# Optimization experiments

Hardware: AMD Instinct MI355X
Metric: run time of the kernel (lower is better)

## Reference

```python
import math
import jax, jax.numpy as jnp
import numpy as np

B, S, G, D = 16, 256, 2048, 512
H = 8
DK = D // H  # per-head key dim
E = 8        # num experts
TOPK = 2


def setup_inputs() -> dict:
    key = jax.random.key(0)
    ks = jax.random.split(key, 12)
    init = lambda k, shape, fan_in: jax.random.uniform(k, shape, jnp.float32, -1.0, 1.0) / np.sqrt(fan_in)
    return {
        'query': jax.random.normal(ks[0], (B, S, D), jnp.float32),
        'key': jax.random.normal(ks[1], (B, G, D), jnp.float32),
        'value': jax.random.normal(ks[2], (B, G, D), jnp.float32),  # unused by module (MHA uses h=key)
        'logit_key': jax.random.normal(ks[3], (B, G, D), jnp.float32),
        'attn_mask': jnp.zeros((B, G), dtype=bool),
        'Wq': init(ks[4], (H, D, DK), D),
        'Wk': init(ks[5], (H, D, DK), D),
        'Wv': init(ks[6], (H, D, DK), D),
        'Wo': init(ks[7], (H, DK, D), DK),
        'w_gate': jnp.zeros((D, E), jnp.float32) + init(ks[8], (D, E), D) * 0.0 + init(ks[9], (D, E), D),
        'expert_w': init(ks[10], (E, D, D), D),
    }


def _mha_glimpse(query, h, attn_mask, Wq, Wk, Wv, Wo):
    # Kool-style MHA: K and V both derived from h
    Q = jnp.einsum('bsd,hdk->bhsk', query, Wq)
    K = jnp.einsum('bgd,hdk->bhgk', h, Wk)
    V = jnp.einsum('bgd,hdk->bhgk', h, Wv)
    scores = jnp.einsum('bhsk,bhgk->bhsg', Q, K) / math.sqrt(DK)
    # 2D mask (B,G) expanded over heads and steps; True = masked out
    mask = attn_mask[:, None, None, :]
    scores = jnp.where(mask, jnp.float32(-1e9), scores)
    attn = jax.nn.softmax(scores, axis=-1)
    heads = jnp.einsum('bhsg,bhgk->bhsk', attn, V)
    return jnp.einsum('bhsk,hkd->bsd', heads, Wo)


def _moe(x, w_gate, expert_w):
    # x: (N, D). Noisy top-k gating, eval mode (no noise): clean logits -> top-k -> softmax over top-k.
    logits = x @ w_gate                                  # (N, E)
    top_vals, top_idx = jax.lax.top_k(logits, TOPK)      # (N, k)
    top_gates = jax.nn.softmax(top_vals, axis=-1)        # (N, k)
    gates = jnp.sum(jax.nn.one_hot(top_idx, E, dtype=x.dtype) * top_gates[..., None], axis=1)  # (N, E)
    expert_out = jnp.einsum('nd,edo->neo', x, expert_w)  # dense combine: same math as dispatch/scatter
    return jnp.einsum('ne,neo->no', gates, expert_out)


def reference(query, key, value, logit_key, attn_mask, Wq, Wk, Wv, Wo, w_gate, expert_w):
    glimpse = _mha_glimpse(query, key, attn_mask, Wq, Wk, Wv, Wo)  # (B, S, D)
    gm = _moe(glimpse.reshape(B * S, D), w_gate, expert_w).reshape(B, S, D)
    logits = jnp.einsum('bsd,bgd->bsg', gm, logit_key) / math.sqrt(D)
    return logits
```

## Files before the change

kernel.cpp:

```cpp
#include <hip/hip_runtime.h>

#define B_  16
#define S_  256
#define G_  2048
#define D_  512
#define H_  8
#define DK_ 64
#define E_  8

typedef _Float16 half8  __attribute__((ext_vector_type(8)));
typedef _Float16 half4v __attribute__((ext_vector_type(4)));
typedef float    floatx4 __attribute__((ext_vector_type(4)));
typedef float    floatx16 __attribute__((ext_vector_type(16)));

#define GLDS(g, l) __builtin_amdgcn_global_load_lds( \
    (const __attribute__((address_space(1))) void*)(g), \
    (__attribute__((address_space(3))) void*)(l), 16, 0, 0)

__global__ void __launch_bounds__(256) split_f16(
    const float* __restrict__ src, _Float16* __restrict__ hi,
    _Float16* __restrict__ lo, int n4)
{
    int i = blockIdx.x * 256 + threadIdx.x;
    if (i >= n4) return;
    float4 v = ((const float4*)src)[i];
    half4v h, l;
    h[0] = (_Float16)v.x; h[1] = (_Float16)v.y;
    h[2] = (_Float16)v.z; h[3] = (_Float16)v.w;
    l[0] = (_Float16)(v.x - (float)h[0]); l[1] = (_Float16)(v.y - (float)h[1]);
    l[2] = (_Float16)(v.z - (float)h[2]); l[3] = (_Float16)(v.w - (float)h[3]);
    ((half4v*)hi)[i] = h;
    ((half4v*)lo)[i] = l;
}

__global__ void __launch_bounds__(256) transpose_split(
    const float* __restrict__ src, _Float16* __restrict__ hi,
    _Float16* __restrict__ lo, int R, int C)
{
    __shared__ float T[32][33];
    const int tid = threadIdx.x;
    const long zo = (long)blockIdx.z * R * C;
    const int r0 = blockIdx.y * 32, c0 = blockIdx.x * 32;
#pragma unroll
    for (int p = 0; p < 4; ++p) {
        int i = tid + p * 256;
        int lr = i >> 5, lc = i & 31;
        T[lr][lc] = src[zo + (long)(r0 + lr) * C + (c0 + lc)];
    }
    __syncthreads();
#pragma unroll
    for (int p = 0; p < 4; ++p) {
        int i = tid + p * 256;
        int orr = i >> 5, oc = i & 31;
        float v = T[oc][orr];
        _Float16 h = (_Float16)v;
        long o = zo + (long)(c0 + orr) * R + (r0 + oc);
        hi[o] = h;
        lo[o] = (_Float16)(v - (float)h);
    }
}

__global__ void __launch_bounds__(256) mask_bitmap(
    const unsigned char* __restrict__ mask, unsigned long long* __restrict__ bmp)
{
    const int t = blockIdx.x * 256 + threadIdx.x;
    const int b = t >> 5, tile = t & 31;
    const unsigned long long* m8 =
        (const unsigned long long*)(mask + (long)b * G_ + tile * 64);
    unsigned long long v = 0ULL;
#pragma unroll
    for (int i = 0; i < 8; ++i) {
        const unsigned long long w = m8[i];
#pragma unroll
        for (int j = 0; j < 8; ++j)
            v |= (((w >> (8 * j)) & 0xFFULL) ? 1ULL : 0ULL) << (8 * i + j);
    }
    bmp[t] = v;
}

__global__ void __launch_bounds__(256) gemm_f16x3(
    const _Float16* __restrict__ Ah, const _Float16* __restrict__ Al,
    const _Float16* __restrict__ Bh, const _Float16* __restrict__ Bl,
    float* __restrict__ C, _Float16* __restrict__ Chi, _Float16* __restrict__ Clo,
    long ldc, long sAz, long sBz, long sCz, float alpha)
{
    __shared__ _Float16 Ash[128 * 32], Asl[128 * 32];
    __shared__ _Float16 Bsh[128 * 32], Bsl[128 * 32];
    const int tid = threadIdx.x;
    const int w = tid >> 6, lane = tid & 63;
    const int quad = lane >> 4, tn = lane & 15;
    const int wm = (w >> 1) * 64, wn = (w & 1) * 64;
    const int z = blockIdx.z;
    const long m0 = (long)blockIdx.y * 128;
    const long n0 = (long)blockIdx.x * 128;
    const _Float16* Agh = Ah + (z * sAz + m0) * 512;
    const _Float16* Agl = Al + (z * sAz + m0) * 512;
    const _Float16* Bgh = Bh + (z * sBz + n0) * 512;
    const _Float16* Bgl = Bl + (z * sBz + n0) * 512;
    const long glane = (long)(lane >> 2) * 512 + (lane & 3) * 8;

    floatx4 acc[4][4] = {};

    for (int k0 = 0; k0 < 512; k0 += 32) {
#pragma unroll
        for (int cc = 0; cc < 2; ++cc) {
            const int c = 2 * w + cc;
            const long go = (long)c * 16 * 512 + glane + k0;
            GLDS(Agh + go, Ash + c * 512);
            GLDS(Agl + go, Asl + c * 512);
            GLDS(Bgh + go, Bsh + c * 512);
            GLDS(Bgl + go, Bsl + c * 512);
        }
        asm volatile("s_waitcnt vmcnt(0)" ::: "memory");
        __syncthreads();

        half8 ah[4], al[4], bh[4], bl[4];
#pragma unroll
        for (int t = 0; t < 4; ++t) {
            ah[t] = *(const half8*)&Ash[(wm + t * 16 + tn) * 32 + quad * 8];
            al[t] = *(const half8*)&Asl[(wm + t * 16 + tn) * 32 + quad * 8];
            bh[t] = *(const half8*)&Bsh[(wn + t * 16 + tn) * 32 + quad * 8];
            bl[t] = *(const half8*)&Bsl[(wn + t * 16 + tn) * 32 + quad * 8];
        }
#pragma unroll
        for (int i = 0; i < 4; ++i)
#pragma unroll
            for (int j = 0; j < 4; ++j) {
                acc[i][j] = __builtin_amdgcn_mfma_f32_16x16x32_f16(ah[i], bh[j], acc[i][j], 0, 0, 0);
                acc[i][j] = __builtin_amdgcn_mfma_f32_16x16x32_f16(ah[i], bl[j], acc[i][j], 0, 0, 0);
                acc[i][j] = __builtin_amdgcn_mfma_f32_16x16x32_f16(al[i], bh[j], acc[i][j], 0, 0, 0);
            }
        __syncthreads();
    }

#pragma unroll
    for (int i = 0; i < 4; ++i) {
        const long row0 = m0 + wm + i * 16 + quad * 4;
#pragma unroll
        for (int r = 0; r < 4; ++r) {
            const long row = row0 + r;
#pragma unroll
            for (int j = 0; j < 4; ++j) {
                float v = acc[i][j][r] * alpha;
                const long o = (long)z * sCz + row * ldc + n0 + wn + j * 16 + tn;
                if (C) C[o] = v;
                if (Chi) {
                    _Float16 hh = (_Float16)v;
                    Chi[o] = hh;
                    Clo[o] = (_Float16)(v - (float)hh);
                }
            }
        }
    }
}

__global__ void __launch_bounds__(256) flash_mfma(
    const _Float16* __restrict__ qh, const _Float16* __restrict__ qlo,
    const _Float16* __restrict__ kh, const _Float16* __restrict__ kl,
    const _Float16* __restrict__ vh, const _Float16* __restrict__ vl,
    const unsigned long long* __restrict__ bmp,
    float* __restrict__ Opart, float* __restrict__ Lpart)
{
    __shared__ half8 KH[512], KL[512], VH[512], VL[512];
    const int tid = threadIdx.x;
    const int wid = tid >> 6, lane = tid & 63;
    const int lh = lane >> 5, ln = lane & 31;
    const int head = blockIdx.y, b = blockIdx.z;
    const int sblk = blockIdx.x & 1, gq = blockIdx.x >> 1;
    const long tok0 = (long)b * S_ + sblk * 128 + wid * 32;

    const long qoff = (tok0 + ln) * 512 + head * 64 + lh * 8;
    half8 qfh[4], qfl[4];
#pragma unroll
    for (int ks = 0; ks < 4; ++ks) {
        qfh[ks] = *(const half8*)(qh + qoff + ks * 16);
        qfl[ks] = *(const half8*)(qlo + qoff + ks * 16);
    }

    const int srow_lo = lane >> 3;
    const int sgs = lane & 7;
    const long kgK = (long)b * G_ * 512 + head * 64;
    const long kgV = (long)head * 64 * (B_ * G_) + (long)b * G_;

    floatx16 accO[2] = {};
    float lsum = 0.f;

    for (int t = 0; t < 8; ++t) {
        const int g0 = gq * 512 + t * 64;
#pragma unroll
        for (int cc = 0; cc < 2; ++cc) {
            const int c = 2 * wid + cc;
            const int r = c * 8 + srow_lo;
            const int gs = sgs ^ (r & 7);
            const long ko = kgK + (long)(g0 + r) * 512 + gs * 8;
            const long vo = kgV + (long)r * (B_ * G_) + g0 + gs * 8;
            GLDS(kh + ko, KH + c * 64);
            GLDS(kl + ko, KL + c * 64);
            GLDS(vh + vo, VH + c * 64);
            GLDS(vl + vo, VL + c * 64);
        }
        asm volatile("s_waitcnt vmcnt(0)" ::: "memory");
        __syncthreads();

        floatx16 accS[2] = {};
#pragma unroll
        for (int gt = 0; gt < 2; ++gt) {
            const int grow = gt * 32 + ln;
            const int gbase = grow * 8, gswz = grow & 7;
#pragma unroll
            for (int ks = 0; ks < 4; ++ks) {
                const int gi = gbase + ((ks * 2 + lh) ^ gswz);
                half8 kbh = KH[gi], kbl = KL[gi];
                accS[gt] = __builtin_amdgcn_mfma_f32_32x32x16_f16(kbh, qfh[ks], accS[gt], 0, 0, 0);
                accS[gt] = __builtin_amdgcn_mfma_f32_32x32x16_f16(kbh, qfl[ks], accS[gt], 0, 0, 0);
                accS[gt] = __builtin_amdgcn_mfma_f32_32x32x16_f16(kbl, qfh[ks], accS[gt], 0, 0, 0);
            }
        }

        const unsigned long long bm = bmp[(b << 5) + (g0 >> 6)];
        if (bm != 0ULL) {
            const unsigned w0 = lh ? ((unsigned)bm >> 4) : (unsigned)bm;
            const unsigned w1 = lh ? ((unsigned)(bm >> 32) >> 4) : (unsigned)(bm >> 32);
#pragma unroll
            for (int gt = 0; gt < 2; ++gt) {
                const unsigned wsel = gt ? w1 : w0;
#pragma unroll
                for (int r = 0; r < 16; ++r) {
                    const int sh = (r & 3) + 8 * (r >> 2);
                    if ((wsel >> sh) & 1u) accS[gt][r] = -1.0e9f;
                }
            }
        }

        float rs = 0.f;
#pragma unroll
        for (int gt = 0; gt < 2; ++gt)
#pragma unroll
            for (int r = 0; r < 16; ++r) {
                const float pv = __builtin_exp2f(accS[gt][r]);
                accS[gt][r] = pv;
                rs += pv;
            }
        rs += __shfl_xor(rs, 32);
        lsum += rs;

#pragma unroll
        for (int gt = 0; gt < 2; ++gt)
#pragma unroll
            for (int w = 0; w < 2; ++w) {
                half8 ph, pl;
#pragma unroll
                for (int j = 0; j < 4; ++j) {
                    const float pA = accS[gt][8 * w + j];
                    const float pB = accS[gt][8 * w + 4 + j];
                    const float snd = lh ? pA : pB;
                    const float rcv = __shfl_xor(snd, 32);
                    const float e03 = lh ? rcv : pA;
                    const float e47 = lh ? pB : rcv;
                    float hi = __uint_as_float(__float_as_uint(e03) & 0xFFFFE000u);
                    ph[j] = (_Float16)hi;
                    pl[j] = (_Float16)(e03 - hi);
                    hi = __uint_as_float(__float_as_uint(e47) & 0xFFFFE000u);
                    ph[4 + j] = (_Float16)hi;
                    pl[4 + j] = (_Float16)(e47 - hi);
                }
                const int gvb = gt * 4 + w * 2 + lh;
#pragma unroll
                for (int nt = 0; nt < 2; ++nt) {
                    const int vrow = nt * 32 + ln;
                    const int gi = vrow * 8 + (gvb ^ (vrow & 7));
                    half8 vbh = VH[gi], vbl = VL[gi];
                    accO[nt] = __builtin_amdgcn_mfma_f32_32x32x16_f16(ph, vbh, accO[nt], 0, 0, 0);
                    accO[nt] = __builtin_amdgcn_mfma_f32_32x32x16_f16(ph, vbl, accO[nt], 0, 0, 0);
                    accO[nt] = __builtin_amdgcn_mfma_f32_32x32x16_f16(pl, vbh, accO[nt], 0, 0, 0);
                }
            }
        __syncthreads();
    }

    float* Op = Opart + (long)gq * (4096L * 512);
#pragma unroll
    for (int nt = 0; nt < 2; ++nt)
#pragma unroll
        for (int r = 0; r < 16; ++r) {
            const int s = (r & 3) + 8 * (r >> 2) + 4 * lh;
            Op[(tok0 + s) * 512 + head * 64 + nt * 32 + ln] = accO[nt][r];
        }
    if (lane < 32)
        Lpart[(long)gq * 32768 + (tok0 + lane) * 8 + head] = lsum;
}

__global__ void __launch_bounds__(256) combine_flash(
    const float* __restrict__ Op, const float* __restrict__ Lp,
    _Float16* __restrict__ hd_hi, _Float16* __restrict__ hd_lo)
{
    const int idx = blockIdx.x * 256 + threadIdx.x;
    const int n = idx >> 7;
    const int c = (idx & 127) * 4;
    const int h = c >> 6;
    float l = 0.f;
#pragma unroll
    for (int q = 0; q < 4; ++q) l += Lp[q * 32768 + (long)n * 8 + h];
    const float inv = 1.0f / l;
    float4 a = *(const float4*)(Op + (long)n * 512 + c);
#pragma unroll
    for (int q = 1; q < 4; ++q) {
        float4 d = *(const float4*)(Op + (long)q * 2097152 + (long)n * 512 + c);
        a.x += d.x; a.y += d.y; a.z += d.z; a.w += d.w;
    }
    const float ox = a.x * inv, oy = a.y * inv, oz = a.z * inv, ow = a.w * inv;
    half4v hh, ll;
    hh[0] = (_Float16)ox; hh[1] = (_Float16)oy;
    hh[2] = (_Float16)oz; hh[3] = (_Float16)ow;
    ll[0] = (_Float16)(ox - (float)hh[0]); ll[1] = (_Float16)(oy - (float)hh[1]);
    ll[2] = (_Float16)(oz - (float)hh[2]); ll[3] = (_Float16)(ow - (float)hh[3]);
    *(half4v*)(hd_hi + (long)n * 512 + c) = hh;
    *(half4v*)(hd_lo + (long)n * 512 + c) = ll;
}

__global__ void __launch_bounds__(256) gate_topk(
    const _Float16* __restrict__ Xh, const _Float16* __restrict__ Xl,
    const float* __restrict__ wg, float* __restrict__ gates)
{
    __shared__ float W[512][8];
    __shared__ float Xs[64][37];
    const int tid = threadIdx.x;
    const int n0 = blockIdx.x * 64;
#pragma unroll
    for (int p = 0; p < 16; ++p) ((float*)W)[tid + p * 256] = wg[tid + p * 256];

    float acc[8] = {};
    for (int dc = 0; dc < 512; dc += 32) {
        __syncthreads();
#pragma unroll
        for (int p = 0; p < 2; ++p) {
            int f = tid + p * 256;
            int row = f >> 3, c4 = f & 7;
            long o = (long)(n0 + row) * 512 + dc + 4 * c4;
            half4v hv = *(const half4v*)(Xh + o);
            half4v lv = *(const half4v*)(Xl + o);
#pragma unroll
            for (int i = 0; i < 4; ++i) Xs[row][4 * c4 + i] = (float)hv[i] + (float)lv[i];
        }
        __syncthreads();
        if (tid < 64) {
            for (int d2 = 0; d2 < 32; ++d2) {
                float xv = Xs[tid][d2];
#pragma unroll
                for (int e = 0; e < 8; ++e) acc[e] += xv * W[dc + d2][e];
            }
        }
    }
    if (tid < 64) {
        float v1 = -3.0e38f; int i1 = 0;
#pragma unroll
        for (int e = 0; e < 8; ++e) if (acc[e] > v1) { v1 = acc[e]; i1 = e; }
        float v2 = -3.0e38f; int i2 = -1;
#pragma unroll
        for (int e = 0; e < 8; ++e) if (e != i1 && acc[e] > v2) { v2 = acc[e]; i2 = e; }
        float t = __expf(v2 - v1);
        float g1 = 1.0f / (1.0f + t);
        float g2 = t / (1.0f + t);
#pragma unroll
        for (int e = 0; e < 8; ++e)
            gates[(long)(n0 + tid) * 8 + e] = (e == i1) ? g1 : ((e == i2) ? g2 : 0.0f);
    }
}

__global__ void __launch_bounds__(256) combine_moe(
    const float* __restrict__ eo, const float* __restrict__ gates,
    _Float16* __restrict__ gh, _Float16* __restrict__ gl)
{
    const int idx = blockIdx.x * 256 + threadIdx.x;
    const int n = idx >> 7;
    const int c = (idx & 127) * 4;
    float g[8];
#pragma unroll
    for (int e = 0; e < 8; ++e) g[e] = gates[(long)n * 8 + e];
    float ax = 0.f, ay = 0.f, az = 0.f, aw = 0.f;
#pragma unroll
    for (int e = 0; e < 8; ++e) {
        if (g[e] != 0.0f) {
            float4 v = *(const float4*)(eo + (long)e * 2097152 + (long)n * 512 + c);
            ax += g[e] * v.x; ay += g[e] * v.y; az += g[e] * v.z; aw += g[e] * v.w;
        }
    }
    half4v h, l;
    h[0] = (_Float16)ax; h[1] = (_Float16)ay; h[2] = (_Float16)az; h[3] = (_Float16)aw;
    l[0] = (_Float16)(ax - (float)h[0]); l[1] = (_Float16)(ay - (float)h[1]);
    l[2] = (_Float16)(az - (float)h[2]); l[3] = (_Float16)(aw - (float)h[3]);
    *(half4v*)(gh + (long)n * 512 + c) = h;
    *(half4v*)(gl + (long)n * 512 + c) = l;
}

extern "C" void kernel_launch(void* const* d_in, const int* in_sizes, int n_in,
                              void* d_out, int out_size, void* d_ws, size_t ws_size,
                              hipStream_t stream) {
    const float* query     = (const float*)d_in[0];
    const float* key       = (const float*)d_in[1];
    const float* logit_key = (const float*)d_in[3];
    const unsigned char* mask = (const unsigned char*)d_in[4];
    const float* Wq = (const float*)d_in[5];
    const float* Wk = (const float*)d_in[6];
    const float* Wv = (const float*)d_in[7];
    const float* Wo = (const float*)d_in[8];
    const float* wg = (const float*)d_in[9];
    const float* Ew = (const float*)d_in[10];
    float* out = (float*)d_out;

    const size_t MBy = 1048576;
    char* W = (char*)d_ws;
    _Float16* q_hi  = (_Float16*)(W + 0 * MBy);
    _Float16* q_lo  = (_Float16*)(W + 4 * MBy);
    _Float16* kp_hi = (_Float16*)(W + 8 * MBy);
    _Float16* kp_lo = (_Float16*)(W + 40 * MBy);
    _Float16* vt_hi = (_Float16*)(W + 72 * MBy);
    _Float16* vt_lo = (_Float16*)(W + 104 * MBy);
    _Float16* kin_hi = (_Float16*)(W + 136 * MBy);
    _Float16* kin_lo = (_Float16*)(W + 168 * MBy);
    float*    Opart = (float*)(W + 136 * MBy);
    float*    Lpart = (float*)(W + 168 * MBy);
    float*    eo    = (float*)(W + 136 * MBy);
    _Float16* lk_hi = (_Float16*)(W + 136 * MBy);
    _Float16* lk_lo = (_Float16*)(W + 168 * MBy);
    _Float16* wq_hi = (_Float16*)(W + 204 * MBy);
    _Float16* wq_lo = (_Float16*)(W + 204 * MBy + 524288);
    _Float16* wk_hi = (_Float16*)(W + 205 * MBy);
    _Float16* wk_lo = (_Float16*)(W + 205 * MBy + 524288);
    _Float16* wv_hi = (_Float16*)(W + 206 * MBy);
    _Float16* wv_lo = (_Float16*)(W + 206 * MBy + 524288);
    _Float16* wo_hi = (_Float16*)(W + 207 * MBy);
    _Float16* wo_lo = (_Float16*)(W + 207 * MBy + 524288);
    _Float16* ew_hi = (_Float16*)(W + 208 * MBy);
    _Float16* ew_lo = (_Float16*)(W + 212 * MBy);
    _Float16* qi_hi = (_Float16*)(W + 216 * MBy);
    _Float16* qi_lo = (_Float16*)(W + 220 * MBy);
    _Float16* hd_hi = (_Float16*)(W + 216 * MBy);
    _Float16* hd_lo = (_Float16*)(W + 220 * MBy);
    _Float16* gl_hi = (_Float16*)(W + 224 * MBy);
    _Float16* gl_lo = (_Float16*)(W + 228 * MBy);
    _Float16* gm_hi = (_Float16*)(W + 232 * MBy);
    _Float16* gm_lo = (_Float16*)(W + 236 * MBy);
    float*    gates = (float*)(W + 240 * MBy);
    unsigned long long* bmp = (unsigned long long*)(W + 240 * MBy + 131072);

    dim3 blk(256);

    split_f16<<<dim3(16384), blk, 0, stream>>>(key, kin_hi, kin_lo, 4194304);
    split_f16<<<dim3(2048), blk, 0, stream>>>(query, qi_hi, qi_lo, 524288);
    mask_bitmap<<<dim3(2), blk, 0, stream>>>(mask, bmp);
    transpose_split<<<dim3(2, 16, 8), blk, 0, stream>>>(Wq, wq_hi, wq_lo, 512, 64);
    transpose_split<<<dim3(2, 16, 8), blk, 0, stream>>>(Wk, wk_hi, wk_lo, 512, 64);
    transpose_split<<<dim3(2, 16, 8), blk, 0, stream>>>(Wv, wv_hi, wv_lo, 512, 64);
    transpose_split<<<dim3(16, 16, 1), blk, 0, stream>>>(Wo, wo_hi, wo_lo, 512, 512);
    transpose_split<<<dim3(16, 16, 8), blk, 0, stream>>>(Ew, ew_hi, ew_lo, 512, 512);

    gemm_f16x3<<<dim3(4, 32, 1), blk, 0, stream>>>(
        qi_hi, qi_lo, wq_hi, wq_lo, nullptr, q_hi, q_lo, 512, 0, 0, 0,
        0.1803368801111204f);
    gemm_f16x3<<<dim3(4, 256, 1), blk, 0, stream>>>(
        kin_hi, kin_lo, wk_hi, wk_lo, nullptr, kp_hi, kp_lo, 512, 0, 0, 0, 1.0f);
    gemm_f16x3<<<dim3(256, 4, 1), blk, 0, stream>>>(
        wv_hi, wv_lo, kin_hi, kin_lo, nullptr, vt_hi, vt_lo, (long)B_ * G_,
        0, 0, 0, 1.0f);

    flash_mfma<<<dim3(8, H_, B_), blk, 0, stream>>>(
        q_hi, q_lo, kp_hi, kp_lo, vt_hi, vt_lo, bmp, Opart, Lpart);
    combine_flash<<<dim3(2048), blk, 0, stream>>>(Opart, Lpart, hd_hi, hd_lo);

    gemm_f16x3<<<dim3(4, 32, 1), blk, 0, stream>>>(
        hd_hi, hd_lo, wo_hi, wo_lo, nullptr, gl_hi, gl_lo, 512, 0, 0, 0, 1.0f);

    gate_topk<<<dim3(64), blk, 0, stream>>>(gl_hi, gl_lo, wg, gates);

    gemm_f16x3<<<dim3(4, 32, 8), blk, 0, stream>>>(
        gl_hi, gl_lo, ew_hi, ew_lo, eo, nullptr, nullptr, 512, 0, 512, 2097152, 1.0f);

    combine_moe<<<dim3(2048), blk, 0, stream>>>(eo, gates, gm_hi, gm_lo);

    split_f16<<<dim3(16384), blk, 0, stream>>>(logit_key, lk_hi, lk_lo, 4194304);

    gemm_f16x3<<<dim3(16, 2, 16), blk, 0, stream>>>(
        gm_hi, gm_lo, lk_hi, lk_lo, out, nullptr, nullptr, 2048,
        256, 2048, 524288, 0.04419417382415922f);
}
```

Measured before the change: 604.7 us.

## Switch split-f16 GEMM to 32x32x16 MFMA with XOR-swizzled LDS layout

Reworks the gemm_f16x3 inner loop to use 32x32x16 MFMA tiles (2x2 per wave) instead of 16x16x32 tiles (4x4), adjusting fragment loads and the output index mapping to match. The global-to-LDS copy now XOR-swizzles the 16-byte slots by row so that LDS fragment reads avoid bank conflicts. The aim is fewer MFMA instructions, better operand reuse and less LDS conflict stalling, at the cost of a more complex index layout that has to stay consistent between loads and stores.

```diff
diff --git a/kernel.cpp b/kernel.cpp
--- a/kernel.cpp
+++ b/kernel.cpp
@@ -88,7 +88,7 @@
     __shared__ _Float16 Bsh[128 * 32], Bsl[128 * 32];
     const int tid = threadIdx.x;
     const int w = tid >> 6, lane = tid & 63;
-    const int quad = lane >> 4, tn = lane & 15;
+    const int lh = lane >> 5, ln = lane & 31;
     const int wm = (w >> 1) * 64, wn = (w & 1) * 64;
     const int z = blockIdx.z;
     const long m0 = (long)blockIdx.y * 128;
@@ -97,15 +97,18 @@
     const _Float16* Agl = Al + (z * sAz + m0) * 512;
     const _Float16* Bgh = Bh + (z * sBz + n0) * 512;
     const _Float16* Bgl = Bl + (z * sBz + n0) * 512;
-    const long glane = (long)(lane >> 2) * 512 + (lane & 3) * 8;
-
-    floatx4 acc[4][4] = {};
+
+    const int rowc = lane >> 2, slot = lane & 3;
+
+    floatx16 acc[2][2] = {};
 
     for (int k0 = 0; k0 < 512; k0 += 32) {
 #pragma unroll
         for (int cc = 0; cc < 2; ++cc) {
             const int c = 2 * w + cc;
-            const long go = (long)c * 16 * 512 + glane + k0;
+            const int trow = c * 16 + rowc;
+            const int g = slot ^ ((trow >> 1) & 3);
+            const long go = (long)trow * 512 + k0 + g * 8;
             GLDS(Agh + go, Ash + c * 512);
             GLDS(Agl + go, Asl + c * 512);
             GLDS(Bgh + go, Bsh + c * 512);
@@ -114,35 +117,42 @@
         asm volatile("s_waitcnt vmcnt(0)" ::: "memory");
         __syncthreads();
 
-        half8 ah[4], al[4], bh[4], bl[4];
-#pragma unroll
-        for (int t = 0; t < 4; ++t) {
-            ah[t] = *(const half8*)&Ash[(wm + t * 16 + tn) * 32 + quad * 8];
-            al[t] = *(const half8*)&Asl[(wm + t * 16 + tn) * 32 + quad * 8];
-            bh[t] = *(const half8*)&Bsh[(wn + t * 16 + tn) * 32 + quad * 8];
-            bl[t] = *(const half8*)&Bsl[(wn + t * 16 + tn) * 32 + quad * 8];
-        }
-#pragma unroll
-        for (int i = 0; i < 4; ++i)
-#pragma unroll
-            for (int j = 0; j < 4; ++j) {
-                acc[i][j] = __builtin_amdgcn_mfma_f32_16x16x32_f16(ah[i], bh[j], acc[i][j], 0, 0, 0);
-                acc[i][j] = __builtin_amdgcn_mfma_f32_16x16x32_f16(ah[i], bl[j], acc[i][j], 0, 0, 0);
-                acc[i][j] = __builtin_amdgcn_mfma_f32_16x16x32_f16(al[i], bh[j], acc[i][j], 0, 0, 0);
-            }
-        __syncthreads();
-    }
-
-#pragma unroll
-    for (int i = 0; i < 4; ++i) {
-        const long row0 = m0 + wm + i * 16 + quad * 4;
-#pragma unroll
-        for (int r = 0; r < 4; ++r) {
-            const long row = row0 + r;
-#pragma unroll
-            for (int j = 0; j < 4; ++j) {
+        half8 a_h[2][2], a_l[2][2], b_h[2][2], b_l[2][2];
+#pragma unroll
+        for (int i = 0; i < 2; ++i)
+#pragma unroll
+            for (int kk = 0; kk < 2; ++kk) {
+                const int ra = wm + i * 32 + ln;
+                const int sa = (kk * 2 + lh) ^ ((ra >> 1) & 3);
+                a_h[i][kk] = *(const half8*)&Ash[ra * 32 + sa * 8];
+                a_l[i][kk] = *(const half8*)&Asl[ra * 32 + sa * 8];
+                const int rb = wn + i * 32 + ln;
+                const int sb = (kk * 2 + lh) ^ ((rb >> 1) & 3);
+                b_h[i][kk] = *(const half8*)&Bsh[rb * 32 + sb * 8];
+                b_l[i][kk] = *(const half8*)&Bsl[rb * 32 + sb * 8];
+            }
+#pragma unroll
+        for (int i = 0; i < 2; ++i)
+#pragma unroll
+            for (int j = 0; j < 2; ++j)
+#pragma unroll
+                for (int kk = 0; kk < 2; ++kk) {
+                    acc[i][j] = __builtin_amdgcn_mfma_f32_32x32x16_f16(a_h[i][kk], b_h[j][kk], acc[i][j], 0, 0, 0);
+                    acc[i][j] = __builtin_amdgcn_mfma_f32_32x32x16_f16(a_h[i][kk], b_l[j][kk], acc[i][j], 0, 0, 0);
+                    acc[i][j] = __builtin_amdgcn_mfma_f32_32x32x16_f16(a_l[i][kk], b_h[j][kk], acc[i][j], 0, 0, 0);
+                }
+        __syncthreads();
+    }
+
+#pragma unroll
+    for (int i = 0; i < 2; ++i)
+#pragma unroll
+        for (int r = 0; r < 16; ++r) {
+            const long row = m0 + wm + i * 32 + (r & 3) + 8 * (r >> 2) + 4 * lh;
+#pragma unroll
+            for (int j = 0; j < 2; ++j) {
                 float v = acc[i][j][r] * alpha;
-                const long o = (long)z * sCz + row * ldc + n0 + wn + j * 16 + tn;
+                const long o = (long)z * sCz + row * ldc + n0 + wn + j * 32 + ln;
                 if (C) C[o] = v;
                 if (Chi) {
                     _Float16 hh = (_Float16)v;
@@ -151,7 +161,6 @@
                 }
             }
         }
-    }
 }
 
 __global__ void __launch_bounds__(256) flash_mfma(
```

Result: slower. 628.1 us (+3.9%).

## Double-buffer LDS tiles in the split-f16 GEMM to overlap loads with MFMA

Applied to the files above, without the earlier changes.

The split-precision GEMM now keeps two LDS buffers per operand. It issues the global-to-LDS loads for the next K-slice right after the barrier, then runs the MFMAs on the current slice. This drops the trailing barrier per iteration and lets global memory latency hide behind compute. In exchange the kernel uses twice as much LDS per block, which can lower occupancy.

```diff
diff --git a/kernel.cpp b/kernel.cpp
--- a/kernel.cpp
+++ b/kernel.cpp
@@ -84,8 +84,8 @@
     float* __restrict__ C, _Float16* __restrict__ Chi, _Float16* __restrict__ Clo,
     long ldc, long sAz, long sBz, long sCz, float alpha)
 {
-    __shared__ _Float16 Ash[128 * 32], Asl[128 * 32];
-    __shared__ _Float16 Bsh[128 * 32], Bsl[128 * 32];
+    __shared__ _Float16 Ash[2][128 * 32], Asl[2][128 * 32];
+    __shared__ _Float16 Bsh[2][128 * 32], Bsl[2][128 * 32];
     const int tid = threadIdx.x;
     const int w = tid >> 6, lane = tid & 63;
     const int quad = lane >> 4, tn = lane & 15;
@@ -99,28 +99,34 @@
     const _Float16* Bgl = Bl + (z * sBz + n0) * 512;
     const long glane = (long)(lane >> 2) * 512 + (lane & 3) * 8;
 
+#define STAGE_G(buf, kk0) do { \
+    _Pragma("unroll") \
+    for (int cc = 0; cc < 2; ++cc) { \
+        const int c = 2 * w + cc; \
+        const long go = (long)c * 16 * 512 + glane + (kk0); \
+        GLDS(Agh + go, &Ash[buf][c * 512]); \
+        GLDS(Agl + go, &Asl[buf][c * 512]); \
+        GLDS(Bgh + go, &Bsh[buf][c * 512]); \
+        GLDS(Bgl + go, &Bsl[buf][c * 512]); \
+    } } while (0)
+
+    STAGE_G(0, 0);
+
     floatx4 acc[4][4] = {};
 
     for (int k0 = 0; k0 < 512; k0 += 32) {
-#pragma unroll
-        for (int cc = 0; cc < 2; ++cc) {
-            const int c = 2 * w + cc;
-            const long go = (long)c * 16 * 512 + glane + k0;
-            GLDS(Agh + go, Ash + c * 512);
-            GLDS(Agl + go, Asl + c * 512);
-            GLDS(Bgh + go, Bsh + c * 512);
-            GLDS(Bgl + go, Bsl + c * 512);
-        }
+        const int cur = (k0 >> 5) & 1;
         asm volatile("s_waitcnt vmcnt(0)" ::: "memory");
         __syncthreads();
+        if (k0 + 32 < 512) STAGE_G(cur ^ 1, k0 + 32);
 
         half8 ah[4], al[4], bh[4], bl[4];
 #pragma unroll
         for (int t = 0; t < 4; ++t) {
-            ah[t] = *(const half8*)&Ash[(wm + t * 16 + tn) * 32 + quad * 8];
-            al[t] = *(const half8*)&Asl[(wm + t * 16 + tn) * 32 + quad * 8];
-            bh[t] = *(const half8*)&Bsh[(wn + t * 16 + tn) * 32 + quad * 8];
-            bl[t] = *(const half8*)&Bsl[(wn + t * 16 + tn) * 32 + quad * 8];
+            ah[t] = *(const half8*)&Ash[cur][(wm + t * 16 + tn) * 32 + quad * 8];
+            al[t] = *(const half8*)&Asl[cur][(wm + t * 16 + tn) * 32 + quad * 8];
+            bh[t] = *(const half8*)&Bsh[cur][(wn + t * 16 + tn) * 32 + quad * 8];
+            bl[t] = *(const half8*)&Bsl[cur][(wn + t * 16 + tn) * 32 + quad * 8];
         }
 #pragma unroll
         for (int i = 0; i < 4; ++i)
@@ -130,8 +136,8 @@
                 acc[i][j] = __builtin_amdgcn_mfma_f32_16x16x32_f16(ah[i], bl[j], acc[i][j], 0, 0, 0);
                 acc[i][j] = __builtin_amdgcn_mfma_f32_16x16x32_f16(al[i], bh[j], acc[i][j], 0, 0, 0);
             }
-        __syncthreads();
-    }
+    }
+#undef STAGE_G
 
 #pragma unroll
     for (int i = 0; i < 4; ++i) {
```

New measurement: 595.8 us. No clear change (-1.5%).
